# Kernel tuning notes

Measured on AMD Instinct MI355X. Metric: run time of the kernel, lower is better.

Reference implementation:

```python
import jax, jax.numpy as jnp
import numpy as np

N = 50000
E = 800000
H = 4
C = 64
EPS = 1e-5

def _gat_layer(x, W, a_src, a_dst, bias, src, dst, n):
    # x: [N, F_in]; W: [F_in, H*C]
    h = (x @ W).reshape(n, H, C)                      # [N,H,C]
    asrc = jnp.einsum('nhc,hc->nh', h, a_src)         # [N,H]
    adst = jnp.einsum('nhc,hc->nh', h, a_dst)         # [N,H]
    e = jax.nn.leaky_relu(asrc[src] + adst[dst], 0.2) # [E,H]
    emax = jax.ops.segment_max(e, dst, num_segments=n)
    e = jnp.exp(e - emax[dst])
    denom = jax.ops.segment_sum(e, dst, num_segments=n)
    alpha = e / (denom[dst] + 1e-16)                  # [E,H]
    msg = h[src] * alpha[:, :, None]                  # [E,H,C]
    out = jax.ops.segment_sum(msg, dst, num_segments=n)
    return out.reshape(n, H * C) + bias

def _bn_eval(x, gamma, beta, mean, var):
    return (x - mean) * jax.lax.rsqrt(var + EPS) * gamma + beta

def setup_inputs() -> dict:
    key = jax.random.key(0)
    ks = jax.random.split(key, 12)
    d = {}
    d['x'] = jax.random.normal(ks[0], (N, 128), jnp.float32)
    d['edge_index'] = jax.random.randint(ks[1], (2, E), 0, N, jnp.int32)
    d['W1'] = jax.random.normal(ks[2], (128, H * C), jnp.float32) * 0.05
    d['a_src1'] = jax.random.normal(ks[3], (H, C), jnp.float32) * 0.05
    d['a_dst1'] = jax.random.normal(ks[4], (H, C), jnp.float32) * 0.05
    d['b1'] = jnp.zeros((H * C,), jnp.float32)
    d['g1'] = jax.random.uniform(ks[5], (H * C,), jnp.float32, 0.5, 1.5)
    d['be1'] = jnp.zeros((H * C,), jnp.float32)
    d['m1'] = jnp.zeros((H * C,), jnp.float32)
    d['v1'] = jax.random.uniform(ks[6], (H * C,), jnp.float32, 0.5, 1.5)
    d['W2'] = jax.random.normal(ks[7], (H * C, H * C), jnp.float32) * 0.05
    d['a_src2'] = jax.random.normal(ks[8], (H, C), jnp.float32) * 0.05
    d['a_dst2'] = jax.random.normal(ks[9], (H, C), jnp.float32) * 0.05
    d['b2'] = jnp.zeros((H * C,), jnp.float32)
    d['g2'] = jax.random.uniform(ks[10], (H * C,), jnp.float32, 0.5, 1.5)
    d['be2'] = jnp.zeros((H * C,), jnp.float32)
    d['m2'] = jnp.zeros((H * C,), jnp.float32)
    d['v2'] = jax.random.uniform(ks[11], (H * C,), jnp.float32, 0.5, 1.5)
    return d

def reference(x, edge_index, W1, a_src1, a_dst1, b1, g1, be1, m1, v1,
              W2, a_src2, a_dst2, b2, g2, be2, m2, v2):
    # PyG GATConv default: add self-loops
    loops = jnp.arange(N, dtype=edge_index.dtype)
    src = jnp.concatenate([edge_index[0], loops])
    dst = jnp.concatenate([edge_index[1], loops])
    h = _gat_layer(x, W1, a_src1, a_dst1, b1, src, dst, N)
    h = jax.nn.relu(_bn_eval(h, g1, be1, m1, v1))  # dropout identity at eval
    h = _gat_layer(h, W2, a_src2, a_dst2, b2, src, dst, N)
    h = jax.nn.relu(_bn_eval(h, g2, be2, m2, v2))
    return jax.nn.log_softmax(h, axis=1)
```

## Files before the change

kernel.cpp:

```cpp
#include <hip/hip_runtime.h>
#include <hip/hip_bf16.h>
#include <cstdint>

#define N_NODES 50000
#define N_EDGES 800000
#define ET_EDGES (N_EDGES + N_NODES)
#define FDIM 256
#define BN_EPS 1e-5f
#define CAP 96

typedef short bf16x8 __attribute__((ext_vector_type(8)));
typedef float f32x4 __attribute__((ext_vector_type(4)));

__device__ __forceinline__ float lrelu(float x) { return x >= 0.f ? x : 0.2f * x; }
__device__ __forceinline__ unsigned short f2b(float f) {
    unsigned int u = __float_as_uint(f);
    u += 0x7fffu + ((u >> 16) & 1u);
    return (unsigned short)(u >> 16);
}

__device__ __forceinline__ void acc_u8(float acc8[8], int2 p, float c) {
    unsigned px = (unsigned)p.x, py = (unsigned)p.y;
#pragma unroll
    for (int k = 0; k < 4; ++k)
        acc8[k] = fmaf((float)((unsigned char)(px >> (8 * k))), c, acc8[k]);
#pragma unroll
    for (int k = 0; k < 4; ++k)
        acc8[k + 4] = fmaf((float)((unsigned char)(py >> (8 * k))), c, acc8[k + 4]);
}

#define NB_CONV2 3125
#define NB_WT1  128
#define NB_WT2  256
#define SETUP_B (NB_CONV2 + NB_WT1 + NB_WT2 + 1)
#define SCAT_B  3321
__global__ __launch_bounds__(256) void setup_scatter_kernel(
        const float* __restrict__ x, unsigned short* __restrict__ xb,
        const float* __restrict__ W1, unsigned short* __restrict__ W1T,
        const float* __restrict__ W2, unsigned short* __restrict__ W2T,
        const int* __restrict__ ei, int* __restrict__ cursor, int* __restrict__ csr,
        const float* __restrict__ b1, const float* __restrict__ g1,
        const float* __restrict__ be1, const float* __restrict__ m1,
        const float* __restrict__ v1,
        const float* __restrict__ b2, const float* __restrict__ g2,
        const float* __restrict__ be2, const float* __restrict__ m2,
        const float* __restrict__ v2,
        float* sc1, float* sh1, float* sc2, float* sh2) {
    int b = blockIdx.x, tid = threadIdx.x;
    if (b < 2 * SCAT_B && (b & 1)) {
        int e = (b >> 1) * 256 + tid;
        if (e >= ET_EDGES) return;
        int s, d;
        if (e < N_EDGES) { s = ei[e]; d = ei[N_EDGES + e]; }
        else             { s = d = e - N_EDGES; }
        int pos = atomicAdd(&cursor[d], 1);
        if (pos < CAP) csr[d * CAP + pos] = s;
        return;
    }
    int sb = (b < 2 * SCAT_B) ? (b >> 1) : (b - SCAT_B);
    if (sb < NB_CONV2) {
        int i = sb * 512 + tid;
#pragma unroll
        for (int u = 0; u < 2; ++u, i += 256) {
            float4 v = ((const float4*)x)[i];
            ushort4 o;
            o.x = f2b(v.x); o.y = f2b(v.y); o.z = f2b(v.z); o.w = f2b(v.w);
            ((ushort4*)xb)[i] = o;
        }
    } else if (sb < NB_CONV2 + NB_WT1) {
        int t = (sb - NB_CONV2) * 256 + tid;
        int n = t >> 7, k = t & 127;
        W1T[t] = f2b(W1[(size_t)k * 256 + n]);
    } else if (sb < NB_CONV2 + NB_WT1 + NB_WT2) {
        int t = (sb - NB_CONV2 - NB_WT1) * 256 + tid;
        int n = t >> 8, k = t & 255;
        W2T[t] = f2b(W2[(size_t)k * 256 + n]);
    } else {
        int f = tid;
        float s1 = rsqrtf(v1[f] + BN_EPS) * g1[f];
        sc1[f] = s1;
        sh1[f] = (b1[f] - m1[f]) * s1 + be1[f];
        float s2 = rsqrtf(v2[f] + BN_EPS) * g2[f];
        sc2[f] = s2;
        sh2[f] = (b2[f] - m2[f]) * s2 + be2[f];
    }
}

template <int K>
__global__ __launch_bounds__(256) void gemm_fused_kernel(
        const unsigned short* __restrict__ A,
        const unsigned short* __restrict__ BT,
        const float* __restrict__ a_src, const float* __restrict__ a_dst,
        signed char* __restrict__ H8, float* __restrict__ scaleRow,
        float* __restrict__ asrc, float* __restrict__ adst, int M) {
    constexpr int BK = 64;
    __shared__ unsigned short As[64][BK + 8];
    __shared__ unsigned short Bs[256][BK + 8];
    __shared__ int amaxL[64];
    const int tid = threadIdx.x;
    const int lane = tid & 63;
    const int w = tid >> 6;
    const int bm = blockIdx.x * 64;
    const int wc = w * 64;
    const int hd = w;
    if (tid < 64) amaxL[tid] = 0;

    f32x4 acc[4][4];
#pragma unroll
    for (int i = 0; i < 4; ++i)
#pragma unroll
        for (int j = 0; j < 4; ++j) acc[i][j] = (f32x4){0.f, 0.f, 0.f, 0.f};

    const int srow = tid >> 3;
    const int skc = (tid & 7) * 8;

    for (int k0 = 0; k0 < K; k0 += BK) {
#pragma unroll
        for (int i = 0; i < 2; ++i) {
            int row = i * 32 + srow;
            int ar = bm + row; if (ar >= M) ar = M - 1;
            *(bf16x8*)&As[row][skc] = *(const bf16x8*)(A + (size_t)ar * K + k0 + skc);
        }
#pragma unroll
        for (int i = 0; i < 8; ++i) {
            int row = i * 32 + srow;
            *(bf16x8*)&Bs[row][skc] = *(const bf16x8*)(BT + (size_t)row * K + k0 + skc);
        }
        __syncthreads();
#pragma unroll
        for (int ks = 0; ks < BK; ks += 32) {
            const int kk = ks + (lane >> 4) * 8;
            bf16x8 af[4], bfr[4];
#pragma unroll
            for (int i = 0; i < 4; ++i) {
                af[i]  = *(const bf16x8*)&As[i * 16 + (lane & 15)][kk];
                bfr[i] = *(const bf16x8*)&Bs[wc + i * 16 + (lane & 15)][kk];
            }
#pragma unroll
            for (int i = 0; i < 4; ++i)
#pragma unroll
                for (int j = 0; j < 4; ++j)
                    acc[i][j] = __builtin_amdgcn_mfma_f32_16x16x32_bf16(af[i], bfr[j], acc[i][j], 0, 0, 0);
        }
        __syncthreads();
    }

    const int q = lane >> 4, c16 = lane & 15;
#pragma unroll
    for (int i = 0; i < 4; ++i) {
#pragma unroll
        for (int r = 0; r < 4; ++r) {
            float a = fmaxf(fmaxf(fabsf(acc[i][0][r]), fabsf(acc[i][1][r])),
                            fmaxf(fabsf(acc[i][2][r]), fabsf(acc[i][3][r])));
#pragma unroll
            for (int off = 1; off < 16; off <<= 1) a = fmaxf(a, __shfl_xor(a, off));
            if (c16 == 0) atomicMax(&amaxL[i * 16 + q * 4 + r], __float_as_int(a));
        }
    }
    __syncthreads();

    float asv[4], adv[4];
#pragma unroll
    for (int j = 0; j < 4; ++j) {
        int c = j * 16 + c16;
        asv[j] = a_src[hd * 64 + c];
        adv[j] = a_dst[hd * 64 + c];
    }
#pragma unroll
    for (int i = 0; i < 4; ++i) {
#pragma unroll
        for (int r = 0; r < 4; ++r) {
            int lrow = i * 16 + q * 4 + r;
            int gr = bm + lrow;
            float amax = __int_as_float(amaxL[lrow]);
            float rcpS = amax > 1e-20f ? 127.f / amax : 0.f;
            if (gr < M) {
#pragma unroll
                for (int j = 0; j < 4; ++j) {
                    int qv = (int)rintf(acc[i][j][r] * rcpS);
                    H8[(size_t)gr * 256 + wc + j * 16 + c16] =
                        (signed char)(unsigned char)(qv + 128);
                }
                if (c16 == 0 && w == 0) scaleRow[gr] = amax * (1.f / 127.f);
            }
            float p_s = acc[i][0][r] * asv[0] + acc[i][1][r] * asv[1]
                      + acc[i][2][r] * asv[2] + acc[i][3][r] * asv[3];
            float p_d = acc[i][0][r] * adv[0] + acc[i][1][r] * adv[1]
                      + acc[i][2][r] * adv[2] + acc[i][3][r] * adv[3];
#pragma unroll
            for (int off = 1; off < 16; off <<= 1) {
                p_s += __shfl_xor(p_s, off);
                p_d += __shfl_xor(p_d, off);
            }
            if (c16 == 0 && gr < M) {
                asrc[(size_t)gr * 4 + hd] = p_s;
                adst[(size_t)gr * 4 + hd] = p_d;
            }
        }
    }
}

template <bool FINAL>
__device__ __forceinline__ void gat_epilogue(const float acc8[8], int fl, bool doStore,
                                             int node, const float* __restrict__ scale,
                                             const float* __restrict__ shift,
                                             float* __restrict__ outf,
                                             unsigned short* __restrict__ outb) {
    float4 scA = ((const float4*)scale)[fl * 2], scB = ((const float4*)scale)[fl * 2 + 1];
    float4 shA = ((const float4*)shift)[fl * 2], shB = ((const float4*)shift)[fl * 2 + 1];
    float t[8];
    t[0] = fmaxf(fmaf(acc8[0], scA.x, shA.x), 0.f);
    t[1] = fmaxf(fmaf(acc8[1], scA.y, shA.y), 0.f);
    t[2] = fmaxf(fmaf(acc8[2], scA.z, shA.z), 0.f);
    t[3] = fmaxf(fmaf(acc8[3], scA.w, shA.w), 0.f);
    t[4] = fmaxf(fmaf(acc8[4], scB.x, shB.x), 0.f);
    t[5] = fmaxf(fmaf(acc8[5], scB.y, shB.y), 0.f);
    t[6] = fmaxf(fmaf(acc8[6], scB.z, shB.z), 0.f);
    t[7] = fmaxf(fmaf(acc8[7], scB.w, shB.w), 0.f);
    if (FINAL) {
        float m = t[0];
#pragma unroll
        for (int k = 1; k < 8; ++k) m = fmaxf(m, t[k]);
#pragma unroll
        for (int off = 1; off < 32; off <<= 1) m = fmaxf(m, __shfl_xor(m, off));
        float es = 0.f;
#pragma unroll
        for (int k = 0; k < 8; ++k) es += __expf(t[k] - m);
#pragma unroll
        for (int off = 1; off < 32; off <<= 1) es += __shfl_xor(es, off);
        float lse = m + logf(es);
        if (doStore) {
            float* p = outf + (size_t)node * 256 + fl * 8;
            *(float4*)p = make_float4(t[0] - lse, t[1] - lse, t[2] - lse, t[3] - lse);
            *(float4*)(p + 4) = make_float4(t[4] - lse, t[5] - lse, t[6] - lse, t[7] - lse);
        }
    } else {
        if (doStore) {
            bf16x8 ob;
#pragma unroll
            for (int k = 0; k < 8; ++k) ob[k] = (short)f2b(t[k]);
            *(bf16x8*)(outb + (size_t)node * 256 + fl * 8) = ob;
        }
    }
}

template <bool FINAL>
__global__ __launch_bounds__(256) void gat_gather_kernel(
        const int* __restrict__ cursor,
        const int* __restrict__ csr,
        const float* __restrict__ asrc,
        const float* __restrict__ adst,
        const float* __restrict__ scaleRow,
        const signed char* __restrict__ h8,
        const float* __restrict__ scale,
        const float* __restrict__ shift,
        float* __restrict__ outf,
        unsigned short* __restrict__ outb) {
    __shared__ int2 sa[4][4][65];

    const int wid = threadIdx.x >> 6;
    const int lane = threadIdx.x & 63;
    const int g = lane >> 5, l32 = lane & 31;
    const int hsel = l32 >> 3;
    const unsigned fo = (unsigned)(l32 << 3);

    const int nodeBase = blockIdx.x * 8 + wid * 2;
    if (nodeBase >= N_NODES) return;

    {
        int node = nodeBase + g;
        bool valid = node < N_NODES;
        int nodeC = valid ? node : N_NODES - 1;
        int deg = valid ? min(cursor[nodeC], CAP) : 0;
        int beg = nodeC * CAP;
        int dmax = max(deg, __shfl_xor(deg, 32));

        if (dmax <= 32) {
            float4 ad = *(const float4*)(adst + (size_t)nodeC * 4);
            int s = 0;
            float sc = 0.f;
            float c0 = -3.4e38f, c1 = -3.4e38f, c2 = -3.4e38f, c3 = -3.4e38f;
            if (l32 < deg) {
                s = csr[beg + l32];
                sc = scaleRow[s];
                float4 as = *(const float4*)(asrc + (size_t)s * 4);
                c0 = lrelu(as.x + ad.x); c1 = lrelu(as.y + ad.y);
                c2 = lrelu(as.z + ad.z); c3 = lrelu(as.w + ad.w);
            }
            float m0 = c0, m1 = c1, m2 = c2, m3 = c3;
#pragma unroll
            for (int off = 1; off < 32; off <<= 1) {
                m0 = fmaxf(m0, __shfl_xor(m0, off)); m1 = fmaxf(m1, __shfl_xor(m1, off));
                m2 = fmaxf(m2, __shfl_xor(m2, off)); m3 = fmaxf(m3, __shfl_xor(m3, off));
            }
            float e0 = 0.f, e1 = 0.f, e2 = 0.f, e3 = 0.f;
            if (l32 < deg) {
                e0 = __expf(c0 - m0); e1 = __expf(c1 - m1);
                e2 = __expf(c2 - m2); e3 = __expf(c3 - m3);
            }
            float s0 = e0, s1 = e1, s2 = e2, s3 = e3;
#pragma unroll
            for (int off = 1; off < 32; off <<= 1) {
                s0 += __shfl_xor(s0, off); s1 += __shfl_xor(s1, off);
                s2 += __shfl_xor(s2, off); s3 += __shfl_xor(s3, off);
            }
            float a0 = e0 / (s0 + 1e-16f) * sc, a1 = e1 / (s1 + 1e-16f) * sc;
            float a2 = e2 / (s2 + 1e-16f) * sc, a3 = e3 / (s3 + 1e-16f) * sc;
            sa[wid][0][lane] = make_int2(s, __float_as_int(a0));
            sa[wid][1][lane] = make_int2(s, __float_as_int(a1));
            sa[wid][2][lane] = make_int2(s, __float_as_int(a2));
            sa[wid][3][lane] = make_int2(s, __float_as_int(a3));
            float t0 = a0, t1 = a1, t2 = a2, t3 = a3;
#pragma unroll
            for (int off = 1; off < 32; off <<= 1) {
                t0 += __shfl_xor(t0, off); t1 += __shfl_xor(t1, off);
                t2 += __shfl_xor(t2, off); t3 += __shfl_xor(t3, off);
            }
            float corr = 128.f * (hsel == 0 ? t0 : hsel == 1 ? t1 : hsel == 2 ? t2 : t3);
            __asm__ volatile("s_waitcnt lgkmcnt(0)" ::: "memory");

            const int2* sal = &sa[wid][hsel][g * 32];
            float acc8[8];
#pragma unroll
            for (int k = 0; k < 8; ++k) acc8[k] = 0.f;

            int e = 0;
            for (; e + 7 < deg; e += 8) {
                int2 sv[8]; int2 hv[8];
#pragma unroll
                for (int u = 0; u < 8; ++u) sv[u] = sal[e + u];
#pragma unroll
                for (int u = 0; u < 8; ++u)
                    hv[u] = *(const int2*)(h8 + (((unsigned)sv[u].x << 8) + fo));
#pragma unroll
                for (int u = 0; u < 8; ++u) acc_u8(acc8, hv[u], __int_as_float(sv[u].y));
            }
            for (; e + 3 < deg; e += 4) {
                int2 sv[4]; int2 hv[4];
#pragma unroll
                for (int u = 0; u < 4; ++u) sv[u] = sal[e + u];
#pragma unroll
                for (int u = 0; u < 4; ++u)
                    hv[u] = *(const int2*)(h8 + (((unsigned)sv[u].x << 8) + fo));
#pragma unroll
                for (int u = 0; u < 4; ++u) acc_u8(acc8, hv[u], __int_as_float(sv[u].y));
            }
            for (; e < deg; ++e) {
                int2 sv = sal[e];
                int2 hA = *(const int2*)(h8 + (((unsigned)sv.x << 8) + fo));
                acc_u8(acc8, hA, __int_as_float(sv.y));
            }
#pragma unroll
            for (int k = 0; k < 8; ++k) acc8[k] -= corr;
            gat_epilogue<FINAL>(acc8, l32, valid, node, scale, shift, outf, outb);
            return;
        }
    }

    for (int t = 0; t < 2; ++t) {
        int fnode = nodeBase + t;
        if (fnode >= N_NODES) break;
        int fdeg = min(cursor[fnode], CAP);
        int fbeg = fnode * CAP, fend = fbeg + fdeg;
        float4 ad = *(const float4*)(adst + (size_t)fnode * 4);
        float acc8[8];
#pragma unroll
        for (int k = 0; k < 8; ++k) acc8[k] = 0.f;
        float corr;

        if (fdeg <= 64) {
            int s = 0;
            float sc = 0.f;
            float c0 = -3.4e38f, c1 = -3.4e38f, c2 = -3.4e38f, c3 = -3.4e38f;
            if (lane < fdeg) {
                s = csr[fbeg + lane];
                sc = scaleRow[s];
                float4 as = *(const float4*)(asrc + (size_t)s * 4);
                c0 = lrelu(as.x + ad.x); c1 = lrelu(as.y + ad.y);
                c2 = lrelu(as.z + ad.z); c3 = lrelu(as.w + ad.w);
            }
            float m0 = c0, m1 = c1, m2 = c2, m3 = c3;
#pragma unroll
            for (int off = 1; off < 64; off <<= 1) {
                m0 = fmaxf(m0, __shfl_xor(m0, off)); m1 = fmaxf(m1, __shfl_xor(m1, off));
                m2 = fmaxf(m2, __shfl_xor(m2, off)); m3 = fmaxf(m3, __shfl_xor(m3, off));
            }
            float e0 = 0.f, e1 = 0.f, e2 = 0.f, e3 = 0.f;
            if (lane < fdeg) {
                e0 = __expf(c0 - m0); e1 = __expf(c1 - m1);
                e2 = __expf(c2 - m2); e3 = __expf(c3 - m3);
            }
            float s0 = e0, s1 = e1, s2 = e2, s3 = e3;
#pragma unroll
            for (int off = 1; off < 64; off <<= 1) {
                s0 += __shfl_xor(s0, off); s1 += __shfl_xor(s1, off);
                s2 += __shfl_xor(s2, off); s3 += __shfl_xor(s3, off);
            }
            float a0 = e0 / (s0 + 1e-16f) * sc, a1 = e1 / (s1 + 1e-16f) * sc;
            float a2 = e2 / (s2 + 1e-16f) * sc, a3 = e3 / (s3 + 1e-16f) * sc;
            sa[wid][0][lane] = make_int2(s, __float_as_int(a0));
            sa[wid][1][lane] = make_int2(s, __float_as_int(a1));
            sa[wid][2][lane] = make_int2(s, __float_as_int(a2));
            sa[wid][3][lane] = make_int2(s, __float_as_int(a3));
            float t0 = a0, t1 = a1, t2 = a2, t3 = a3;
#pragma unroll
            for (int off = 1; off < 64; off <<= 1) {
                t0 += __shfl_xor(t0, off); t1 += __shfl_xor(t1, off);
                t2 += __shfl_xor(t2, off); t3 += __shfl_xor(t3, off);
            }
            corr = 128.f * (hsel == 0 ? t0 : hsel == 1 ? t1 : hsel == 2 ? t2 : t3);
            __asm__ volatile("s_waitcnt lgkmcnt(0)" ::: "memory");

            const int2* sal = &sa[wid][hsel][0];
            int e = 0;
            for (; e + 1 < fdeg; e += 2) {
                int2 sv = sal[e + g];
                int2 hA = *(const int2*)(h8 + (((unsigned)sv.x << 8) + fo));
                acc_u8(acc8, hA, __int_as_float(sv.y));
            }
            if (e < fdeg) {
                int idx = e + g;
                int2 sv = sal[idx < fdeg ? idx : 0];
                float aA = idx < fdeg ? __int_as_float(sv.y) : 0.f;
                int2 hA = *(const int2*)(h8 + (((unsigned)sv.x << 8) + fo));
                acc_u8(acc8, hA, aA);
            }
#pragma unroll
            for (int k = 0; k < 8; ++k) acc8[k] += __shfl_xor(acc8[k], 32);
        } else {
            float m0 = -3.4e38f, m1 = -3.4e38f, m2 = -3.4e38f, m3 = -3.4e38f;
            for (int e = fbeg + lane; e < fend; e += 64) {
                int s = csr[e];
                float4 as = *(const float4*)(asrc + (size_t)s * 4);
                m0 = fmaxf(m0, lrelu(as.x + ad.x)); m1 = fmaxf(m1, lrelu(as.y + ad.y));
                m2 = fmaxf(m2, lrelu(as.z + ad.z)); m3 = fmaxf(m3, lrelu(as.w + ad.w));
            }
#pragma unroll
            for (int off = 1; off < 64; off <<= 1) {
                m0 = fmaxf(m0, __shfl_xor(m0, off)); m1 = fmaxf(m1, __shfl_xor(m1, off));
                m2 = fmaxf(m2, __shfl_xor(m2, off)); m3 = fmaxf(m3, __shfl_xor(m3, off));
            }
            float s0 = 0.f, s1 = 0.f, s2 = 0.f, s3 = 0.f;
            for (int e = fbeg + lane; e < fend; e += 64) {
                int s = csr[e];
                float4 as = *(const float4*)(asrc + (size_t)s * 4);
                s0 += __expf(lrelu(as.x + ad.x) - m0); s1 += __expf(lrelu(as.y + ad.y) - m1);
                s2 += __expf(lrelu(as.z + ad.z) - m2); s3 += __expf(lrelu(as.w + ad.w) - m3);
            }
#pragma unroll
            for (int off = 1; off < 64; off <<= 1) {
                s0 += __shfl_xor(s0, off); s1 += __shfl_xor(s1, off);
                s2 += __shfl_xor(s2, off); s3 += __shfl_xor(s3, off);
            }
            float mh = (hsel == 0) ? m0 : (hsel == 1) ? m1 : (hsel == 2) ? m2 : m3;
            float rh = (hsel == 0) ? 1.f / (s0 + 1e-16f) : (hsel == 1) ? 1.f / (s1 + 1e-16f)
                     : (hsel == 2) ? 1.f / (s2 + 1e-16f) : 1.f / (s3 + 1e-16f);
            float adh = (hsel == 0) ? ad.x : (hsel == 1) ? ad.y : (hsel == 2) ? ad.z : ad.w;
            float asumL = 0.f;
            for (int e = fbeg; e < fend; ++e) {
                int s = csr[e];
                float ash = asrc[(size_t)s * 4 + hsel];
                float a = __expf(lrelu(ash + adh) - mh) * rh * scaleRow[s];
                asumL += a;
                int2 hv = *(const int2*)(h8 + (((unsigned)s << 8) + fo));
                acc_u8(acc8, hv, a);
            }
            corr = 128.f * asumL;
        }
#pragma unroll
        for (int k = 0; k < 8; ++k) acc8[k] -= corr;
        gat_epilogue<FINAL>(acc8, l32, g == 0, fnode, scale, shift, outf, outb);
    }
}

extern "C" void kernel_launch(void* const* d_in, const int* in_sizes, int n_in,
                              void* d_out, int out_size, void* d_ws, size_t ws_size,
                              hipStream_t stream) {
    (void)in_sizes; (void)n_in; (void)out_size; (void)ws_size;
    const float* x   = (const float*)d_in[0];
    const int*   ei  = (const int*)d_in[1];
    const float* W1  = (const float*)d_in[2];
    const float* as1 = (const float*)d_in[3];
    const float* ad1 = (const float*)d_in[4];
    const float* b1  = (const float*)d_in[5];
    const float* g1  = (const float*)d_in[6];
    const float* be1 = (const float*)d_in[7];
    const float* m1  = (const float*)d_in[8];
    const float* v1  = (const float*)d_in[9];
    const float* W2  = (const float*)d_in[10];
    const float* as2 = (const float*)d_in[11];
    const float* ad2 = (const float*)d_in[12];
    const float* b2  = (const float*)d_in[13];
    const float* g2  = (const float*)d_in[14];
    const float* be2 = (const float*)d_in[15];
    const float* m2  = (const float*)d_in[16];
    const float* v2  = (const float*)d_in[17];

    float* out = (float*)d_out;
    unsigned short* actb = (unsigned short*)d_out;

    char* base = (char*)d_ws;
    signed char* h8 = (signed char*)base;          base += (size_t)N_NODES * 256;
    float* scaleRow = (float*)base;                base += (size_t)N_NODES * 4;
    unsigned short* xb  = (unsigned short*)base;   base += (size_t)N_NODES * 128 * 2;
    float* asrc = (float*)base;                    base += (size_t)N_NODES * 4 * 4;
    float* adst = (float*)base;                    base += (size_t)N_NODES * 4 * 4;
    float* sc1 = (float*)base;                     base += 1024;
    float* sh1 = (float*)base;                     base += 1024;
    float* sc2 = (float*)base;                     base += 1024;
    float* sh2 = (float*)base;                     base += 1024;
    unsigned short* W1T = (unsigned short*)base;   base += 256 * 128 * 2;
    unsigned short* W2T = (unsigned short*)base;   base += 256 * 256 * 2;
    int* cursor = (int*)base;                      base += N_NODES * 4;
    int* csr  = (int*)base;

    hipMemsetAsync(cursor, 0, (size_t)N_NODES * 4, stream);

    setup_scatter_kernel<<<SETUP_B + SCAT_B, 256, 0, stream>>>(
        x, xb, W1, W1T, W2, W2T, ei, cursor, csr,
        b1, g1, be1, m1, v1, b2, g2, be2, m2, v2, sc1, sh1, sc2, sh2);

    const int gb = (N_NODES + 63) / 64;
    const int nb = (N_NODES + 7) / 8;

    gemm_fused_kernel<128><<<gb, 256, 0, stream>>>(xb, W1T, as1, ad1, h8, scaleRow,
                                                   asrc, adst, N_NODES);
    gat_gather_kernel<false><<<nb, 256, 0, stream>>>(cursor, csr, asrc, adst, scaleRow, h8,
                                                     sc1, sh1, nullptr, actb);

    gemm_fused_kernel<256><<<gb, 256, 0, stream>>>(actb, W2T, as2, ad2, h8, scaleRow,
                                                   asrc, adst, N_NODES);
    gat_gather_kernel<true><<<nb, 256, 0, stream>>>(cursor, csr, asrc, adst, scaleRow, h8,
                                                    sc2, sh2, out, nullptr);
}
```

Measured before the change: 300.7 us.

## Fuse edge scatter with first GEMM and convert x to bf16 inline

Removes the separate fp32-to-bf16 conversion pass over x: the first-layer GEMM now converts x tiles to bf16 while staging them in shared memory. That GEMM is launched in the same grid as the CSR edge scatter, with interleaved block indices, so the atomic-heavy scatter and the MFMA GEMM run concurrently. The cursor memset is folded into the prep kernel, which also does the weight transposes. This saves one kernel launch and a full read and write of the bf16 copy of x, at the cost of fp32 global loads inside the GEMM and a larger mixed-role kernel.

```diff
diff --git a/kernel.cpp b/kernel.cpp
--- a/kernel.cpp
+++ b/kernel.cpp
@@ -29,16 +29,13 @@
         acc8[k + 4] = fmaf((float)((unsigned char)(py >> (8 * k))), c, acc8[k + 4]);
 }
 
-#define NB_CONV2 3125
-#define NB_WT1  128
-#define NB_WT2  256
-#define SETUP_B (NB_CONV2 + NB_WT1 + NB_WT2 + 1)
-#define SCAT_B  3321
-__global__ __launch_bounds__(256) void setup_scatter_kernel(
-        const float* __restrict__ x, unsigned short* __restrict__ xb,
+#define PB_Z  196
+#define PB_W1 128
+#define PB_W2 256
+__global__ __launch_bounds__(256) void prep_kernel(
         const float* __restrict__ W1, unsigned short* __restrict__ W1T,
         const float* __restrict__ W2, unsigned short* __restrict__ W2T,
-        const int* __restrict__ ei, int* __restrict__ cursor, int* __restrict__ csr,
+        int* __restrict__ cursor,
         const float* __restrict__ b1, const float* __restrict__ g1,
         const float* __restrict__ be1, const float* __restrict__ m1,
         const float* __restrict__ v1,
@@ -47,32 +44,15 @@
         const float* __restrict__ v2,
         float* sc1, float* sh1, float* sc2, float* sh2) {
     int b = blockIdx.x, tid = threadIdx.x;
-    if (b < 2 * SCAT_B && (b & 1)) {
-        int e = (b >> 1) * 256 + tid;
-        if (e >= ET_EDGES) return;
-        int s, d;
-        if (e < N_EDGES) { s = ei[e]; d = ei[N_EDGES + e]; }
-        else             { s = d = e - N_EDGES; }
-        int pos = atomicAdd(&cursor[d], 1);
-        if (pos < CAP) csr[d * CAP + pos] = s;
-        return;
-    }
-    int sb = (b < 2 * SCAT_B) ? (b >> 1) : (b - SCAT_B);
-    if (sb < NB_CONV2) {
-        int i = sb * 512 + tid;
-#pragma unroll
-        for (int u = 0; u < 2; ++u, i += 256) {
-            float4 v = ((const float4*)x)[i];
-            ushort4 o;
-            o.x = f2b(v.x); o.y = f2b(v.y); o.z = f2b(v.z); o.w = f2b(v.w);
-            ((ushort4*)xb)[i] = o;
-        }
-    } else if (sb < NB_CONV2 + NB_WT1) {
-        int t = (sb - NB_CONV2) * 256 + tid;
+    if (b < PB_Z) {
+        int i = b * 256 + tid;
+        if (i < N_NODES) cursor[i] = 0;
+    } else if (b < PB_Z + PB_W1) {
+        int t = (b - PB_Z) * 256 + tid;
         int n = t >> 7, k = t & 127;
         W1T[t] = f2b(W1[(size_t)k * 256 + n]);
-    } else if (sb < NB_CONV2 + NB_WT1 + NB_WT2) {
-        int t = (sb - NB_CONV2 - NB_WT1) * 256 + tid;
+    } else if (b < PB_Z + PB_W1 + PB_W2) {
+        int t = (b - PB_Z - PB_W1) * 256 + tid;
         int n = t >> 8, k = t & 255;
         W2T[t] = f2b(W2[(size_t)k * 256 + n]);
     } else {
@@ -83,6 +63,150 @@
         float s2 = rsqrtf(v2[f] + BN_EPS) * g2[f];
         sc2[f] = s2;
         sh2[f] = (b2[f] - m2[f]) * s2 + be2[f];
+    }
+}
+
+#define SG_GEMM 782
+#define SG_SCAT 3321
+#define SG_MIX  (2 * SG_GEMM)
+__global__ __launch_bounds__(256) void scat_gemm1_kernel(
+        const int* __restrict__ ei, int* __restrict__ cursor, int* __restrict__ csr,
+        const float* __restrict__ x,
+        const unsigned short* __restrict__ BT,
+        const float* __restrict__ a_src, const float* __restrict__ a_dst,
+        signed char* __restrict__ H8, float* __restrict__ scaleRow,
+        float* __restrict__ asrc, float* __restrict__ adst, int M) {
+    constexpr int K = 128;
+    constexpr int BK = 64;
+    __shared__ unsigned short As[64][BK + 8];
+    __shared__ unsigned short Bs[256][BK + 8];
+    __shared__ int amaxL[64];
+    const int tid = threadIdx.x;
+    const int b = blockIdx.x;
+
+    int gemmIdx = -1, scatIdx = 0;
+    if (b < SG_MIX) { if (b & 1) gemmIdx = b >> 1; else scatIdx = b >> 1; }
+    else scatIdx = b - SG_GEMM;
+
+    if (gemmIdx < 0) {
+        int e = scatIdx * 256 + tid;
+        if (e < ET_EDGES) {
+            int s, d;
+            if (e < N_EDGES) { s = ei[e]; d = ei[N_EDGES + e]; }
+            else             { s = d = e - N_EDGES; }
+            int pos = atomicAdd(&cursor[d], 1);
+            if (pos < CAP) csr[d * CAP + pos] = s;
+        }
+        return;
+    }
+
+    const int lane = tid & 63;
+    const int w = tid >> 6;
+    const int bm = gemmIdx * 64;
+    const int wc = w * 64;
+    const int hd = w;
+    if (tid < 64) amaxL[tid] = 0;
+
+    f32x4 acc[4][4];
+#pragma unroll
+    for (int i = 0; i < 4; ++i)
+#pragma unroll
+        for (int j = 0; j < 4; ++j) acc[i][j] = (f32x4){0.f, 0.f, 0.f, 0.f};
+
+    const int srow = tid >> 3;
+    const int skc = (tid & 7) * 8;
+
+    for (int k0 = 0; k0 < K; k0 += BK) {
+#pragma unroll
+        for (int i = 0; i < 2; ++i) {
+            int row = i * 32 + srow;
+            int ar = bm + row; if (ar >= M) ar = M - 1;
+            const float* xp = x + (size_t)ar * K + k0 + skc;
+            float4 v0 = *(const float4*)xp;
+            float4 v1 = *(const float4*)(xp + 4);
+            bf16x8 o;
+            o[0] = (short)f2b(v0.x); o[1] = (short)f2b(v0.y);
+            o[2] = (short)f2b(v0.z); o[3] = (short)f2b(v0.w);
+            o[4] = (short)f2b(v1.x); o[5] = (short)f2b(v1.y);
+            o[6] = (short)f2b(v1.z); o[7] = (short)f2b(v1.w);
+            *(bf16x8*)&As[row][skc] = o;
+        }
+#pragma unroll
+        for (int i = 0; i < 8; ++i) {
+            int row = i * 32 + srow;
+            *(bf16x8*)&Bs[row][skc] = *(const bf16x8*)(BT + (size_t)row * K + k0 + skc);
+        }
+        __syncthreads();
+#pragma unroll
+        for (int ks = 0; ks < BK; ks += 32) {
+            const int kk = ks + (lane >> 4) * 8;
+            bf16x8 af[4], bfr[4];
+#pragma unroll
+            for (int i = 0; i < 4; ++i) {
+                af[i]  = *(const bf16x8*)&As[i * 16 + (lane & 15)][kk];
+                bfr[i] = *(const bf16x8*)&Bs[wc + i * 16 + (lane & 15)][kk];
+            }
+#pragma unroll
+            for (int i = 0; i < 4; ++i)
+#pragma unroll
+                for (int j = 0; j < 4; ++j)
+                    acc[i][j] = __builtin_amdgcn_mfma_f32_16x16x32_bf16(af[i], bfr[j], acc[i][j], 0, 0, 0);
+        }
+        __syncthreads();
+    }
+
+    const int q = lane >> 4, c16 = lane & 15;
+#pragma unroll
+    for (int i = 0; i < 4; ++i) {
+#pragma unroll
+        for (int r = 0; r < 4; ++r) {
+            float a = fmaxf(fmaxf(fabsf(acc[i][0][r]), fabsf(acc[i][1][r])),
+                            fmaxf(fabsf(acc[i][2][r]), fabsf(acc[i][3][r])));
+#pragma unroll
+            for (int off = 1; off < 16; off <<= 1) a = fmaxf(a, __shfl_xor(a, off));
+            if (c16 == 0) atomicMax(&amaxL[i * 16 + q * 4 + r], __float_as_int(a));
+        }
+    }
+    __syncthreads();
+
+    float asv[4], adv[4];
+#pragma unroll
+    for (int j = 0; j < 4; ++j) {
+        int c = j * 16 + c16;
+        asv[j] = a_src[hd * 64 + c];
+        adv[j] = a_dst[hd * 64 + c];
+    }
+#pragma unroll
+    for (int i = 0; i < 4; ++i) {
+#pragma unroll
+        for (int r = 0; r < 4; ++r) {
+            int lrow = i * 16 + q * 4 + r;
+            int gr = bm + lrow;
+            float amax = __int_as_float(amaxL[lrow]);
+            float rcpS = amax > 1e-20f ? 127.f / amax : 0.f;
+            if (gr < M) {
+#pragma unroll
+                for (int j = 0; j < 4; ++j) {
+                    int qv = (int)rintf(acc[i][j][r] * rcpS);
+                    H8[(size_t)gr * 256 + wc + j * 16 + c16] =
+                        (signed char)(unsigned char)(qv + 128);
+                }
+                if (c16 == 0 && w == 0) scaleRow[gr] = amax * (1.f / 127.f);
+            }
+            float p_s = acc[i][0][r] * asv[0] + acc[i][1][r] * asv[1]
+                      + acc[i][2][r] * asv[2] + acc[i][3][r] * asv[3];
+            float p_d = acc[i][0][r] * adv[0] + acc[i][1][r] * adv[1]
+                      + acc[i][2][r] * adv[2] + acc[i][3][r] * adv[3];
+#pragma unroll
+            for (int off = 1; off < 16; off <<= 1) {
+                p_s += __shfl_xor(p_s, off);
+                p_d += __shfl_xor(p_d, off);
+            }
+            if (c16 == 0 && gr < M) {
+                asrc[(size_t)gr * 4 + hd] = p_s;
+                adst[(size_t)gr * 4 + hd] = p_d;
+            }
+        }
     }
 }
 
@@ -502,7 +626,7 @@
     char* base = (char*)d_ws;
     signed char* h8 = (signed char*)base;          base += (size_t)N_NODES * 256;
     float* scaleRow = (float*)base;                base += (size_t)N_NODES * 4;
-    unsigned short* xb  = (unsigned short*)base;   base += (size_t)N_NODES * 128 * 2;
+    base += (size_t)N_NODES * 128 * 2;
     float* asrc = (float*)base;                    base += (size_t)N_NODES * 4 * 4;
     float* adst = (float*)base;                    base += (size_t)N_NODES * 4 * 4;
     float* sc1 = (float*)base;                     base += 1024;
@@ -514,22 +638,22 @@
     int* cursor = (int*)base;                      base += N_NODES * 4;
     int* csr  = (int*)base;
 
-    hipMemsetAsync(cursor, 0, (size_t)N_NODES * 4, stream);
-
-    setup_scatter_kernel<<<SETUP_B + SCAT_B, 256, 0, stream>>>(
-        x, xb, W1, W1T, W2, W2T, ei, cursor, csr,
+    prep_kernel<<<PB_Z + PB_W1 + PB_W2 + 1, 256, 0, stream>>>(
+        W1, W1T, W2, W2T, cursor,
         b1, g1, be1, m1, v1, b2, g2, be2, m2, v2, sc1, sh1, sc2, sh2);
 
+    const int nb = (N_NODES + 7) / 8;
     const int gb = (N_NODES + 63) / 64;
-    const int nb = (N_NODES + 7) / 8;
-
-    gemm_fused_kernel<128><<<gb, 256, 0, stream>>>(xb, W1T, as1, ad1, h8, scaleRow,
-                                                   asrc, adst, N_NODES);
+
+    scat_gemm1_kernel<<<SG_SCAT + SG_GEMM, 256, 0, stream>>>(
+        ei, cursor, csr, x, W1T, as1, ad1, h8, scaleRow, asrc, adst, N_NODES);
+
     gat_gather_kernel<false><<<nb, 256, 0, stream>>>(cursor, csr, asrc, adst, scaleRow, h8,
                                                      sc1, sh1, nullptr, actb);
 
     gemm_fused_kernel<256><<<gb, 256, 0, stream>>>(actb, W2T, as2, ad2, h8, scaleRow,
                                                    asrc, adst, N_NODES);
+
     gat_gather_kernel<true><<<nb, 256, 0, stream>>>(cursor, csr, asrc, adst, scaleRow, h8,
                                                     sc2, sh2, out, nullptr);
 }
```

New measurement: 291.1 us (median of 2 runs). -3.2%, faster.
